# Performance work log

Hardware: AMD Instinct MI355X
Metric: run time of the kernel (lower is better)

## Reference

```python
import jax, jax.numpy as jnp
import numpy as np

D_MODEL = 768
NUM_HEADS = 12
D_K = D_MODEL // NUM_HEADS
D_FF = 3072
EPS = 1e-5


def _layer_norm(x, gamma, beta):
    mu = jnp.mean(x, axis=-1, keepdims=True)
    var = jnp.mean(jnp.square(x - mu), axis=-1, keepdims=True)
    return (x - mu) * jax.lax.rsqrt(var + EPS) * gamma + beta


def setup_inputs() -> dict:
    key = jax.random.key(0)
    ks = jax.random.split(key, 16)
    s = 1.0 / np.sqrt(D_MODEL)
    sf = 1.0 / np.sqrt(D_FF)
    inp = {
        "x": jax.random.normal(ks[0], (2, 2048, D_MODEL), dtype=jnp.float32),
        "Wq": jax.random.uniform(ks[1], (D_MODEL, D_MODEL), jnp.float32, -s, s),
        "bq": jax.random.uniform(ks[2], (D_MODEL,), jnp.float32, -s, s),
        "Wk": jax.random.uniform(ks[3], (D_MODEL, D_MODEL), jnp.float32, -s, s),
        "bk": jax.random.uniform(ks[4], (D_MODEL,), jnp.float32, -s, s),
        "Wv": jax.random.uniform(ks[5], (D_MODEL, D_MODEL), jnp.float32, -s, s),
        "bv": jax.random.uniform(ks[6], (D_MODEL,), jnp.float32, -s, s),
        "Wo": jax.random.uniform(ks[7], (D_MODEL, D_MODEL), jnp.float32, -s, s),
        "bo": jax.random.uniform(ks[8], (D_MODEL,), jnp.float32, -s, s),
        "W1": jax.random.uniform(ks[9], (D_MODEL, D_FF), jnp.float32, -s, s),
        "b1": jax.random.uniform(ks[10], (D_FF,), jnp.float32, -s, s),
        "W2": jax.random.uniform(ks[11], (D_FF, D_MODEL), jnp.float32, -sf, sf),
        "b2": jax.random.uniform(ks[12], (D_MODEL,), jnp.float32, -sf, sf),
        "g1": jnp.ones((D_MODEL,), jnp.float32),
        "be1": jnp.zeros((D_MODEL,), jnp.float32),
        "g2": jnp.ones((D_MODEL,), jnp.float32),
        "be2": jnp.zeros((D_MODEL,), jnp.float32),
    }
    return inp


def reference(x, Wq, bq, Wk, bk, Wv, bv, Wo, bo, W1, b1, W2, b2, g1, be1, g2, be2):
    B, S, _ = x.shape

    def split(h):  # (B,S,D) -> (B,H,S,Dk)
        return h.reshape(B, S, NUM_HEADS, D_K).transpose(0, 2, 1, 3)

    q = split(x @ Wq + bq)
    k = split(x @ Wk + bk)
    v = split(x @ Wv + bv)

    # naive attention: materialize full (B,H,S,S) scores as in the original
    scores = jnp.einsum("bhsd,bhtd->bhst", q, k) / np.sqrt(D_K)
    attn = jax.nn.softmax(scores, axis=-1)
    ctx = jnp.einsum("bhst,bhtd->bhsd", attn, v)
    ctx = ctx.transpose(0, 2, 1, 3).reshape(B, S, D_MODEL)
    attn_out = ctx @ Wo + bo

    x = _layer_norm(x + attn_out, g1, be1)
    ff = jax.nn.relu(x @ W1 + b1) @ W2 + b2
    x = _layer_norm(x + ff, g2, be2)
    return x
```

## Files before the change

### kernel.cpp

```cpp
#include <hip/hip_runtime.h>
#include <cstdint>


typedef unsigned short u16;
typedef unsigned int u32;
typedef __attribute__((ext_vector_type(4))) float f32x4;
typedef __attribute__((ext_vector_type(8))) short s16x8;
typedef __attribute__((ext_vector_type(4))) u16  u16x4;
typedef __attribute__((ext_vector_type(2))) u32  u32x2;

#define AS1 __attribute__((address_space(1)))
#define AS3 __attribute__((address_space(3)))

__device__ __forceinline__ u16 f2b(float f) {
  union { float f; unsigned u; } v; v.f = f;
  unsigned r = v.u + 0x7FFFu + ((v.u >> 16) & 1u);
  return (u16)(r >> 16);
}

__device__ __forceinline__ float b2f(u16 v) {
  union { float f; u32 u; } x; x.u = ((u32)v) << 16; return x.f;
}

__device__ __forceinline__ void gl_lds16(const void* g, void* lds_uniform_base) {
  __builtin_amdgcn_global_load_lds((const AS1 void*)g, (AS3 void*)lds_uniform_base, 16, 0, 0);
}

__device__ __forceinline__ f32x4 mfma16(s16x8 a, s16x8 b, f32x4 c) {
  return __builtin_amdgcn_mfma_f32_16x16x32_bf16(a, b, c, 0, 0, 0);
}

__device__ __forceinline__ u32 cvt_pk_bf16(float lo, float hi) {
  u32 r;
  asm("v_cvt_pk_bf16_f32 %0, %1, %2" : "=v"(r) : "v"(lo), "v"(hi));
  return r;
}

__device__ __forceinline__ float max3f(float a, float b, float c) {
  return fmaxf(fmaxf(a, b), c);
}

__device__ __forceinline__ void block_barrier() {
  asm volatile("" ::: "memory");
  __builtin_amdgcn_s_barrier();
  asm volatile("" ::: "memory");
}

__global__ __launch_bounds__(256) void prep(
    const float* __restrict__ Wq, const float* __restrict__ Wk,
    const float* __restrict__ Wv, const float* __restrict__ Wo,
    const float* __restrict__ W1, const float* __restrict__ W2,
    const float* __restrict__ bq, const float* __restrict__ bk,
    const float* __restrict__ bv, const float* __restrict__ x,
    u16* __restrict__ Wqkv_t, u16* __restrict__ Wo_t,
    u16* __restrict__ W1_t, u16* __restrict__ W2_t,
    float* __restrict__ bqkv, u16* __restrict__ Xb, int convBlocks) {
  __shared__ float ts[32][33];
  const int bid = blockIdx.x;
  const int tx = threadIdx.x, ty = threadIdx.y;
  if (bid < 6912) {
    const float* W; u16* Wt; int K, N, tile;
    if (bid < 2304) {
      int w = bid / 576; tile = bid - w * 576; K = 768; N = 768;
      W = (w == 0) ? Wq : (w == 1) ? Wk : (w == 2) ? Wv : Wo;
      Wt = (w < 3) ? Wqkv_t + (size_t)w * 768 * 768 : Wo_t;
    } else if (bid < 4608) {
      tile = bid - 2304; K = 768; N = 3072; W = W1; Wt = W1_t;
    } else {
      tile = bid - 4608; K = 3072; N = 768; W = W2; Wt = W2_t;
    }
    int ntx = N >> 5;
    int n0 = (tile % ntx) * 32, k0 = (tile / ntx) * 32;
#pragma unroll
    for (int yy = 0; yy < 32; yy += 8)
      ts[ty + yy][tx] = W[(size_t)(k0 + ty + yy) * N + n0 + tx];
    __syncthreads();
#pragma unroll
    for (int yy = 0; yy < 32; yy += 8)
      Wt[(size_t)(n0 + ty + yy) * K + k0 + tx] = f2b(ts[tx][ty + yy]);
  } else if (bid < 6912 + convBlocks) {
    int t = ty * 32 + tx;
    size_t i = ((size_t)(bid - 6912) * 256 + t) * 4;
    f32x4 v = *(const f32x4*)(x + i);
    u16x4 o;
#pragma unroll
    for (int k = 0; k < 4; ++k) o[k] = f2b(v[k]);
    *(u16x4*)(Xb + i) = o;
  } else {
    int t = ty * 32 + tx;
    int i = (bid - 6912 - convBlocks) * 256 + t;
    if (i < 2304) bqkv[i] = (i < 768) ? bq[i] : (i < 1536) ? bk[i - 768] : bv[i - 1536];
  }
}

__global__ __launch_bounds__(256) void transpose_v(const u16* __restrict__ Vh,
                                                   u16* __restrict__ Vt) {
  __shared__ u16 tile[32][33];
  int bh = blockIdx.z;
  int d0 = blockIdx.x * 32, s0 = blockIdx.y * 32;
  const u16* src = Vh + (size_t)bh * 2048 * 64;
  u16* dst = Vt + (size_t)bh * 64 * 2048;
  int x = threadIdx.x, y = threadIdx.y;
#pragma unroll
  for (int yy = 0; yy < 32; yy += 8)
    tile[y + yy][x] = src[(size_t)(s0 + y + yy) * 64 + d0 + x];
  __syncthreads();
#pragma unroll
  for (int yy = 0; yy < 32; yy += 8)
    dst[(size_t)(d0 + y + yy) * 2048 + s0 + x] = tile[x][y + yy];
}

template <int MODE>
__global__ __launch_bounds__(256) void gemm_bt(const u16* __restrict__ A,
                                               const u16* __restrict__ Bt,
                                               const float* __restrict__ bias,
                                               float* __restrict__ Cf, u16* __restrict__ Cb,
                                               u16* __restrict__ Qo, u16* __restrict__ Ko,
                                               u16* __restrict__ Vo, int M, int N, int K,
                                               int Klen) {
  __shared__ __align__(16) u16 lsA[2][128 * 64];
  __shared__ __align__(16) u16 lsB[2][128 * 64];
  const int tid = threadIdx.x;
  const int lane = tid & 63, wave = tid >> 6;
  const int lr = lane & 15, lh = lane >> 4;
  const int wr = wave >> 1, wc = wave & 1;

  int bx, by, bz;
  {
    int nx = gridDim.x, ny = gridDim.y, nz = gridDim.z;
    int total = nx * ny * nz;
    int lin = blockIdx.x + nx * (blockIdx.y + ny * blockIdx.z);
    if ((total & 7) == 0) {
      int key = (lin & 7) * (total >> 3) + (lin >> 3);
      by = key % ny;
      int t2 = key / ny;
      bz = t2 % nz;
      bx = t2 / nz;
    } else {
      bx = blockIdx.x; by = blockIdx.y; bz = blockIdx.z;
    }
  }
  const int m0 = by * 128;
  const int n0 = bx * 128;
  const int kB = bz * Klen;

  f32x4 acc[4][4];
#pragma unroll
  for (int i = 0; i < 4; ++i)
#pragma unroll
    for (int j = 0; j < 4; ++j) acc[i][j] = f32x4{0.f, 0.f, 0.f, 0.f};

  const size_t aBase = (size_t)m0 * K;
  const size_t bBase = (size_t)n0 * K;
  const int srow8 = tid >> 3;
  const int scolE = (((tid & 7) * 16) ^ ((srow8 & 7) << 4)) >> 1;
  const int xk = (lr & 7) << 4;

  auto stage = [&](int buf, int kt) {
#pragma unroll
    for (int i = 0; i < 4; ++i) {
      int row = i * 32 + srow8;
      int ldsOff = buf * 16384 + i * 4096 + wave * 1024;
      gl_lds16(A + aBase + (size_t)row * K + kt + scolE, (char*)lsA + ldsOff);
      gl_lds16(Bt + bBase + (size_t)row * K + kt + scolE, (char*)lsB + ldsOff);
    }
  };

  const int nk = Klen >> 6;
  stage(0, kB);
  for (int t = 0; t < nk; ++t) {
    const int cur = t & 1;
    if (t + 1 < nk) {
      stage(cur ^ 1, kB + (t + 1) * 64);
      asm volatile("s_waitcnt vmcnt(8)" ::: "memory");
    } else {
      asm volatile("s_waitcnt vmcnt(0)" ::: "memory");
    }
    block_barrier();
    const char* baA = (const char*)lsA + cur * 16384;
    const char* baB = (const char*)lsB + cur * 16384;
#pragma unroll
    for (int ks = 0; ks < 2; ++ks) {
      int cb = (ks * 64 + lh * 16) ^ xk;
      s16x8 a[4], b[4];
#pragma unroll
      for (int i = 0; i < 4; ++i) {
        a[i] = *(const s16x8*)(baA + (wr * 64 + i * 16 + lr) * 128 + cb);
        b[i] = *(const s16x8*)(baB + (wc * 64 + i * 16 + lr) * 128 + cb);
      }
#pragma unroll
      for (int i = 0; i < 4; ++i)
#pragma unroll
        for (int j = 0; j < 4; ++j) acc[i][j] = mfma16(a[i], b[j], acc[i][j]);
    }
    block_barrier();
  }

  float* CfP = Cf + (size_t)bz * M * N;
#pragma unroll
  for (int i = 0; i < 4; ++i) {
    int growb = m0 + wr * 64 + i * 16 + lh * 4;
#pragma unroll
    for (int j = 0; j < 4; ++j) {
      int col = n0 + wc * 64 + j * 16 + lr;
      float bv = (MODE != 0 || bz == 0) ? bias[col] : 0.f;
#pragma unroll
      for (int q = 0; q < 4; ++q) {
        int grow = growb + q;
        float v = acc[i][j][q] + bv;
        if (MODE == 0) {
          CfP[(size_t)grow * N + col] = v;
        } else if (MODE == 1) {
          Cb[(size_t)grow * N + col] = f2b(fmaxf(v, 0.f));
        } else {
          int sel = col / 768;
          int c2 = col - sel * 768;
          int h = c2 >> 6, d = c2 & 63;
          int b = grow >> 11, s = grow & 2047;
          size_t idx = (((size_t)(b * 12 + h)) * 2048 + s) * 64 + d;
          float vv = (sel == 0) ? v * 0.1803368801f : v;
          u16* dst = (sel == 0) ? Qo : (sel == 1) ? Ko : Vo;
          dst[idx] = f2b(vv);
        }
      }
    }
  }
}

__global__ __launch_bounds__(512) void attn(const u16* __restrict__ Qh,
                                            const u16* __restrict__ Kh,
                                            const u16* __restrict__ Vt,
                                            u16* __restrict__ Opb,
                                            float* __restrict__ ml,
                                            int nbh, int ntile) {
  __shared__ __align__(16) u16 lsK[2][64 * 64];
  __shared__ __align__(16) u16 lsV[2][64 * 64];
  __shared__ __align__(16) u16 lsP[8][16 * 64];
  const int tid = threadIdx.x, lane = tid & 63, wave = tid >> 6;
  const int lr = lane & 15, lh = lane >> 4;

  int bx = blockIdx.x, bh = blockIdx.y, z = blockIdx.z;
  {
    int nz = gridDim.z;
    int total = 16 * nbh * nz;
    if ((total & 7) == 0) {
      int lin = bx + 16 * (bh + nbh * z);
      int nl = (lin & 7) * (total >> 3) + (lin >> 3);
      bx = nl & 15;
      bh = (nl >> 4) % nbh;
      z = nl / (16 * nbh);
    }
  }
  const int q0 = bx * 128 + wave * 16;
  const size_t kvBase = (size_t)bh * 2048 * 64;
  const int tB = z * ntile;

  const int srow = tid >> 3;
  const int scol = (((tid & 7) * 16) ^ ((srow & 7) << 4)) >> 1;
  const u16* kSrcBase = Kh + kvBase + (size_t)srow * 64 + scol;
  const u16* vSrcBase = Vt + kvBase + (size_t)srow * 2048 + scol;

  s16x8 qf[2];
#pragma unroll
  for (int ks = 0; ks < 2; ++ks)
    qf[ks] = *(const s16x8*)(Qh + kvBase + (size_t)(q0 + lr) * 64 + ks * 32 + lh * 8);

  s16x8 onesf;
#pragma unroll
  for (int k = 0; k < 8; ++k) onesf[k] = (short)0x3F80;

  f32x4 oacc[4];
  f32x4 aOnes = f32x4{0.f, 0.f, 0.f, 0.f};
  float mrow = -1e30f;
#pragma unroll
  for (int d = 0; d < 4; ++d) oacc[d] = f32x4{0.f, 0.f, 0.f, 0.f};

  gl_lds16(kSrcBase + (size_t)tB * 4096, (char*)lsK[0] + wave * 1024);
  gl_lds16(vSrcBase + tB * 64,           (char*)lsV[0] + wave * 1024);

  for (int it = 0; it < ntile; ++it) {
    const int cur = it & 1;
    __syncthreads();

    s16x8 kb[2][4];
#pragma unroll
    for (int ks = 0; ks < 2; ++ks)
#pragma unroll
      for (int j = 0; j < 4; ++j) {
        int r = j * 16 + lr;
        kb[ks][j] = *(const s16x8*)((const char*)lsK[cur] + r * 128 +
                                    ((ks * 64 + lh * 16) ^ ((r & 7) << 4)));
      }

    if (it + 1 < ntile) {
      int t = tB + it + 1;
      gl_lds16(kSrcBase + (size_t)t * 4096, (char*)lsK[cur ^ 1] + wave * 1024);
      gl_lds16(vSrcBase + t * 64,           (char*)lsV[cur ^ 1] + wave * 1024);
    }

    f32x4 st[4];
#pragma unroll
    for (int j = 0; j < 4; ++j) st[j] = f32x4{0.f, 0.f, 0.f, 0.f};
    __builtin_amdgcn_s_setprio(1);
#pragma unroll
    for (int ks = 0; ks < 2; ++ks)
#pragma unroll
      for (int j = 0; j < 4; ++j) st[j] = mfma16(kb[ks][j], qf[ks], st[j]);
    __builtin_amdgcn_s_setprio(0);

    float mx;
    {
      float t0 = max3f(st[0][0], st[0][1], st[0][2]);
      float t1 = max3f(st[0][3], st[1][0], st[1][1]);
      float t2 = max3f(st[1][2], st[1][3], st[2][0]);
      float t3 = max3f(st[2][1], st[2][2], st[2][3]);
      float t4 = max3f(st[3][0], st[3][1], st[3][2]);
      mx = fmaxf(max3f(t0, t1, t2), max3f(t3, t4, st[3][3]));
      mx = fmaxf(mx, __shfl_xor(mx, 16));
      mx = fmaxf(mx, __shfl_xor(mx, 32));
    }
    if (__any(mx > mrow + 11.f)) {
      float mn = fmaxf(mrow, mx);
      float al = exp2f(mrow - mn);
      mrow = mn;
#pragma unroll
      for (int q = 0; q < 4; ++q) aOnes[q] *= al;
#pragma unroll
      for (int d = 0; d < 4; ++d)
#pragma unroll
        for (int q = 0; q < 4; ++q) oacc[d][q] *= al;
    }

#pragma unroll
    for (int j = 0; j < 4; ++j) {
      float p0 = exp2f(st[j][0] - mrow);
      float p1 = exp2f(st[j][1] - mrow);
      float p2 = exp2f(st[j][2] - mrow);
      float p3 = exp2f(st[j][3] - mrow);
      u32x2 pk;
      pk.x = cvt_pk_bf16(p0, p1);
      pk.y = cvt_pk_bf16(p2, p3);
      *(u32x2*)((char*)lsP[wave] + lr * 128 + ((j * 32 + lh * 8) ^ ((lr & 7) << 4))) = pk;
    }

    __builtin_amdgcn_s_setprio(1);
#pragma unroll
    for (int ks = 0; ks < 2; ++ks) {
      s16x8 pa = *(const s16x8*)((const char*)lsP[wave] + lr * 128 +
                                 ((ks * 64 + lh * 16) ^ ((lr & 7) << 4)));
      aOnes = mfma16(onesf, pa, aOnes);
#pragma unroll
      for (int d = 0; d < 4; ++d) {
        int r = d * 16 + lr;
        s16x8 vb = *(const s16x8*)((const char*)lsV[cur] + r * 128 +
                                   ((ks * 64 + lh * 16) ^ ((r & 7) << 4)));
        oacc[d] = mfma16(vb, pa, oacc[d]);
      }
    }
    __builtin_amdgcn_s_setprio(0);
  }

  {
    int s = q0 + lr;
    size_t r = ((size_t)z * nbh + bh) * 2048 + s;
#pragma unroll
    for (int d = 0; d < 4; ++d) {
      u32x2 pk;
      pk.x = cvt_pk_bf16(oacc[d][0], oacc[d][1]);
      pk.y = cvt_pk_bf16(oacc[d][2], oacc[d][3]);
      *(u32x2*)(Opb + r * 64 + d * 16 + lh * 4) = pk;
    }
    if (lh == 0) { ml[r * 2] = mrow; ml[r * 2 + 1] = aOnes[0]; }
  }
}

template <int NZ>
__global__ __launch_bounds__(256) void attn_combine(const u16* __restrict__ Opb,
                                                    const float* __restrict__ ml,
                                                    u16* __restrict__ ctx, int nbh) {
  size_t i = (size_t)blockIdx.x * 256 + threadIdx.x;
  int d4 = (int)(i & 15);
  size_t rs = i >> 4;
  size_t zs = (size_t)nbh * 2048;
  float m[NZ], l[NZ];
  float mx = -1e30f;
#pragma unroll
  for (int p = 0; p < NZ; ++p) {
    m[p] = ml[(p * zs + rs) * 2];
    l[p] = ml[(p * zs + rs) * 2 + 1];
    mx = fmaxf(mx, m[p]);
  }
  float wsum = 0.f, a[NZ];
#pragma unroll
  for (int p = 0; p < NZ; ++p) { a[p] = exp2f(m[p] - mx); wsum += l[p] * a[p]; }
  float inv = 1.f / wsum;
  f32x4 o = f32x4{0.f, 0.f, 0.f, 0.f};
#pragma unroll
  for (int p = 0; p < NZ; ++p) {
    u16x4 op = *(const u16x4*)(Opb + (p * zs + rs) * 64 + d4 * 4);
#pragma unroll
    for (int k = 0; k < 4; ++k) o[k] += b2f(op[k]) * a[p];
  }
  int bh = (int)(rs >> 11), s = (int)(rs & 2047);
  int b = bh / 12, h = bh - b * 12;
  u16x4 r;
#pragma unroll
  for (int k = 0; k < 4; ++k) r[k] = f2b(o[k] * inv);
  *(u16x4*)(ctx + ((size_t)(b * 2048 + s)) * 768 + h * 64 + d4 * 4) = r;
}

template <int NP>
__global__ __launch_bounds__(256) void resid_ln(const float* __restrict__ xin,
                                                const float* __restrict__ yp,
                                                size_t pstride,
                                                const float* __restrict__ gamma,
                                                const float* __restrict__ beta,
                                                float* __restrict__ outf,
                                                u16* __restrict__ outb) {
  const int row = blockIdx.x, t = threadIdx.x;
  const size_t base4 = (size_t)row * 192;
  const bool act = t < 192;
  f32x4 v = f32x4{0.f, 0.f, 0.f, 0.f};
  float s = 0.f, s2 = 0.f;
  if (act) {
    v = ((const f32x4*)xin)[base4 + t];
#pragma unroll
    for (int p = 0; p < NP; ++p) {
      f32x4 y = ((const f32x4*)(yp + p * pstride))[base4 + t];
#pragma unroll
      for (int k = 0; k < 4; ++k) v[k] += y[k];
    }
    s = (v[0] + v[1]) + (v[2] + v[3]);
    s2 = (v[0] * v[0] + v[1] * v[1]) + (v[2] * v[2] + v[3] * v[3]);
  }
#pragma unroll
  for (int off = 32; off > 0; off >>= 1) {
    s += __shfl_down(s, off, 64);
    s2 += __shfl_down(s2, off, 64);
  }
  __shared__ float red[8];
  int lane = t & 63, wave = t >> 6;
  if (lane == 0) { red[wave] = s; red[4 + wave] = s2; }
  __syncthreads();
  s = red[0] + red[1] + red[2] + red[3];
  s2 = red[4] + red[5] + red[6] + red[7];
  const float inv = 1.f / 768.f;
  float mu = s * inv;
  float var = fmaxf(s2 * inv - mu * mu, 0.f);
  float rs = rsqrtf(var + 1e-5f);
  if (act) {
    f32x4 g = ((const f32x4*)gamma)[t];
    f32x4 bb = ((const f32x4*)beta)[t];
    f32x4 o;
#pragma unroll
    for (int k = 0; k < 4; ++k) o[k] = (v[k] - mu) * rs * g[k] + bb[k];
    if (outf) ((f32x4*)outf)[base4 + t] = o;
    if (outb) {
      u16x4 ob;
#pragma unroll
      for (int k = 0; k < 4; ++k) ob[k] = f2b(o[k]);
      ((u16x4*)outb)[base4 + t] = ob;
    }
  }
}

extern "C" void kernel_launch(void* const* d_in, const int* in_sizes, int n_in,
                              void* d_out, int out_size, void* d_ws, size_t ws_size,
                              hipStream_t stream) {
  const float* x   = (const float*)d_in[0];
  const float* Wq  = (const float*)d_in[1];
  const float* bq  = (const float*)d_in[2];
  const float* Wk  = (const float*)d_in[3];
  const float* bk  = (const float*)d_in[4];
  const float* Wv  = (const float*)d_in[5];
  const float* bv  = (const float*)d_in[6];
  const float* Wo  = (const float*)d_in[7];
  const float* bo  = (const float*)d_in[8];
  const float* W1  = (const float*)d_in[9];
  const float* b1  = (const float*)d_in[10];
  const float* W2  = (const float*)d_in[11];
  const float* b2  = (const float*)d_in[12];
  const float* g1  = (const float*)d_in[13];
  const float* be1 = (const float*)d_in[14];
  const float* g2  = (const float*)d_in[15];
  const float* be2 = (const float*)d_in[16];
  float* out = (float*)d_out;

  const int M = in_sizes[0] / 768;
  const int B = M / 2048;
  const int nbh = B * 12;

  char* ws = (char*)d_ws;
  size_t off = 0;
  auto alloc = [&](size_t bytes) -> void* {
    void* p = ws + off;
    off += (bytes + 255) & ~(size_t)255;
    return p;
  };
  u16*   Wqkv_t = (u16*)alloc((size_t)2304 * 768 * 2);
  u16*   Wo_t   = (u16*)alloc((size_t)768 * 768 * 2);
  u16*   W1_t   = (u16*)alloc((size_t)3072 * 768 * 2);
  u16*   W2_t   = (u16*)alloc((size_t)768 * 3072 * 2);
  float* bqkv   = (float*)alloc(2304 * 4);
  u16*   Xb     = (u16*)alloc((size_t)M * 768 * 2);
  u16*   Qh     = (u16*)alloc((size_t)M * 768 * 2);
  u16*   Kh     = (u16*)alloc((size_t)M * 768 * 2);
  u16*   Vh     = (u16*)alloc((size_t)M * 768 * 2);
  u16*   Vt     = (u16*)alloc((size_t)M * 768 * 2);

  size_t pstride = (size_t)M * 768;
  size_t fixedRest = pstride * 4  + pstride * 2  +
                     (size_t)M * 3072 * 2  + 4096;
  const int ZSPLIT = 2;
  size_t opElems = (size_t)ZSPLIT * nbh * 2048 * 64;
  size_t attnBytes = opElems * 2 + (size_t)ZSPLIT * nbh * 2048 * 2 * 4;
  size_t reg4 = attnBytes > pstride * 16 ? attnBytes : pstride * 16;
  int FSPLIT;
  size_t regionBytes;
  if (off + reg4 + fixedRest <= ws_size) {
    FSPLIT = 4; regionBytes = reg4;
  } else {
    FSPLIT = 2;
    regionBytes = attnBytes > pstride * 8 ? attnBytes : pstride * 8;
  }
  float* region = (float*)alloc(regionBytes);
  u16*   Opb  = (u16*)region;
  float* ml   = (float*)((char*)region + opElems * 2);
  float* ffnPart  = region;
  float* projPart = (float*)Qh;
  float* x1f  = (float*)alloc(pstride * 4);
  u16*   x1b  = (u16*)alloc(pstride * 2);
  u16*   hb   = (u16*)alloc((size_t)M * 3072 * 2);
  u16*   ctx  = Xb;

  dim3 tb(32, 8);
  const int convBlocks = (M * 768) / 1024;
  prep<<<6912 + convBlocks + 9, tb, 0, stream>>>(
      Wq, Wk, Wv, Wo, W1, W2, bq, bk, bv, x,
      Wqkv_t, Wo_t, W1_t, W2_t, bqkv, Xb, convBlocks);

  gemm_bt<2><<<dim3(2304 / 128, M / 128), 256, 0, stream>>>(
      Xb, Wqkv_t, bqkv, nullptr, nullptr, Qh, Kh, Vh, M, 2304, 768, 768);

  transpose_v<<<dim3(2, 64, nbh), tb, 0, stream>>>(Vh, Vt);

  attn<<<dim3(16, nbh, ZSPLIT), 512, 0, stream>>>(Qh, Kh, Vt, Opb, ml, nbh, 32 / ZSPLIT);
  attn_combine<2><<<nbh * 128, 256, 0, stream>>>(Opb, ml, ctx, nbh);

  gemm_bt<0><<<dim3(768 / 128, M / 128, 2), 256, 0, stream>>>(
      ctx, Wo_t, bo, projPart, nullptr, nullptr, nullptr, nullptr, M, 768, 768, 384);

  resid_ln<2><<<M, 256, 0, stream>>>(x, projPart, pstride, g1, be1, x1f, x1b);

  gemm_bt<1><<<dim3(3072 / 128, M / 128), 256, 0, stream>>>(
      x1b, W1_t, b1, nullptr, hb, nullptr, nullptr, nullptr, M, 3072, 768, 768);

  if (FSPLIT == 4) {
    gemm_bt<0><<<dim3(768 / 128, M / 128, 4), 256, 0, stream>>>(
        hb, W2_t, b2, ffnPart, nullptr, nullptr, nullptr, nullptr, M, 768, 3072, 768);
    resid_ln<4><<<M, 256, 0, stream>>>(x1f, ffnPart, pstride, g2, be2, out, nullptr);
  } else {
    gemm_bt<0><<<dim3(768 / 128, M / 128, 2), 256, 0, stream>>>(
        hb, W2_t, b2, ffnPart, nullptr, nullptr, nullptr, nullptr, M, 768, 3072, 1536);
    resid_ln<2><<<M, 256, 0, stream>>>(x1f, ffnPart, pstride, g2, be2, out, nullptr);
  }
}
```

Baseline: 210.6 us.

## Fuse V transpose into QKV GEMM epilogue and store split-K partials as bf16

The QKV GEMM epilogue now writes V directly in transposed per-head layout as 4-element vector stores, which removes the separate transpose_v kernel and the Vh buffer. The split-K partial outputs of the Wo and W2 GEMMs are stored as bf16 instead of fp32, and resid_ln reads them back as bf16. This halves the partial-sum traffic, at the cost of precision loss in the residual sums.

Result: faster. 202.5 us (median of 2 runs) (-3.8%).

```diff
diff --git a/kernel.cpp b/kernel.cpp
--- a/kernel.cpp
+++ b/kernel.cpp
@@ -93,30 +93,13 @@
   }
 }
 
-__global__ __launch_bounds__(256) void transpose_v(const u16* __restrict__ Vh,
-                                                   u16* __restrict__ Vt) {
-  __shared__ u16 tile[32][33];
-  int bh = blockIdx.z;
-  int d0 = blockIdx.x * 32, s0 = blockIdx.y * 32;
-  const u16* src = Vh + (size_t)bh * 2048 * 64;
-  u16* dst = Vt + (size_t)bh * 64 * 2048;
-  int x = threadIdx.x, y = threadIdx.y;
-#pragma unroll
-  for (int yy = 0; yy < 32; yy += 8)
-    tile[y + yy][x] = src[(size_t)(s0 + y + yy) * 64 + d0 + x];
-  __syncthreads();
-#pragma unroll
-  for (int yy = 0; yy < 32; yy += 8)
-    dst[(size_t)(d0 + y + yy) * 2048 + s0 + x] = tile[x][y + yy];
-}
-
 template <int MODE>
 __global__ __launch_bounds__(256) void gemm_bt(const u16* __restrict__ A,
                                                const u16* __restrict__ Bt,
                                                const float* __restrict__ bias,
-                                               float* __restrict__ Cf, u16* __restrict__ Cb,
+                                               u16* __restrict__ Cb,
                                                u16* __restrict__ Qo, u16* __restrict__ Ko,
-                                               u16* __restrict__ Vo, int M, int N, int K,
+                                               u16* __restrict__ Vt, int M, int N, int K,
                                                int Klen) {
   __shared__ __align__(16) u16 lsA[2][128 * 64];
   __shared__ __align__(16) u16 lsB[2][128 * 64];
@@ -196,7 +179,7 @@
     block_barrier();
   }
 
-  float* CfP = Cf + (size_t)bz * M * N;
+  u16* CbP = Cb + (size_t)bz * M * N;
 #pragma unroll
   for (int i = 0; i < 4; ++i) {
     int growb = m0 + wr * 64 + i * 16 + lh * 4;
@@ -204,23 +187,36 @@
     for (int j = 0; j < 4; ++j) {
       int col = n0 + wc * 64 + j * 16 + lr;
       float bv = (MODE != 0 || bz == 0) ? bias[col] : 0.f;
-#pragma unroll
-      for (int q = 0; q < 4; ++q) {
-        int grow = growb + q;
-        float v = acc[i][j][q] + bv;
-        if (MODE == 0) {
-          CfP[(size_t)grow * N + col] = v;
-        } else if (MODE == 1) {
-          Cb[(size_t)grow * N + col] = f2b(fmaxf(v, 0.f));
+      if (MODE == 2) {
+        int sel = col / 768;
+        int c2 = col - sel * 768;
+        int h = c2 >> 6, d = c2 & 63;
+        int b = growb >> 11, s0 = growb & 2047;
+        if (sel == 2) {
+          u16x4 ob;
+#pragma unroll
+          for (int q = 0; q < 4; ++q) ob[q] = f2b(acc[i][j][q] + bv);
+          *(u16x4*)(Vt + (((size_t)(b * 12 + h)) * 64 + d) * 2048 + s0) = ob;
         } else {
-          int sel = col / 768;
-          int c2 = col - sel * 768;
-          int h = c2 >> 6, d = c2 & 63;
-          int b = grow >> 11, s = grow & 2047;
-          size_t idx = (((size_t)(b * 12 + h)) * 2048 + s) * 64 + d;
-          float vv = (sel == 0) ? v * 0.1803368801f : v;
-          u16* dst = (sel == 0) ? Qo : (sel == 1) ? Ko : Vo;
-          dst[idx] = f2b(vv);
+#pragma unroll
+          for (int q = 0; q < 4; ++q) {
+            float v = acc[i][j][q] + bv;
+            size_t idx = (((size_t)(b * 12 + h)) * 2048 + (s0 + q)) * 64 + d;
+            float vv = (sel == 0) ? v * 0.1803368801f : v;
+            u16* dst = (sel == 0) ? Qo : Ko;
+            dst[idx] = f2b(vv);
+          }
+        }
+      } else {
+#pragma unroll
+        for (int q = 0; q < 4; ++q) {
+          int grow = growb + q;
+          float v = acc[i][j][q] + bv;
+          if (MODE == 0) {
+            CbP[(size_t)grow * N + col] = f2b(v);
+          } else {
+            Cb[(size_t)grow * N + col] = f2b(fmaxf(v, 0.f));
+          }
         }
       }
     }
@@ -411,7 +407,7 @@
 
 template <int NP>
 __global__ __launch_bounds__(256) void resid_ln(const float* __restrict__ xin,
-                                                const float* __restrict__ yp,
+                                                const u16* __restrict__ yp,
                                                 size_t pstride,
                                                 const float* __restrict__ gamma,
                                                 const float* __restrict__ beta,
@@ -426,9 +422,9 @@
     v = ((const f32x4*)xin)[base4 + t];
 #pragma unroll
     for (int p = 0; p < NP; ++p) {
-      f32x4 y = ((const f32x4*)(yp + p * pstride))[base4 + t];
-#pragma unroll
-      for (int k = 0; k < 4; ++k) v[k] += y[k];
+      u16x4 y = *(const u16x4*)(yp + p * pstride + (size_t)row * 768 + t * 4);
+#pragma unroll
+      for (int k = 0; k < 4; ++k) v[k] += b2f(y[k]);
     }
     s = (v[0] + v[1]) + (v[2] + v[3]);
     s2 = (v[0] * v[0] + v[1] * v[1]) + (v[2] * v[2] + v[3] * v[3]);
@@ -505,7 +501,6 @@
   u16*   Xb     = (u16*)alloc((size_t)M * 768 * 2);
   u16*   Qh     = (u16*)alloc((size_t)M * 768 * 2);
   u16*   Kh     = (u16*)alloc((size_t)M * 768 * 2);
-  u16*   Vh     = (u16*)alloc((size_t)M * 768 * 2);
   u16*   Vt     = (u16*)alloc((size_t)M * 768 * 2);
 
   size_t pstride = (size_t)M * 768;
@@ -514,20 +509,21 @@
   const int ZSPLIT = 2;
   size_t opElems = (size_t)ZSPLIT * nbh * 2048 * 64;
   size_t attnBytes = opElems * 2 + (size_t)ZSPLIT * nbh * 2048 * 2 * 4;
-  size_t reg4 = attnBytes > pstride * 16 ? attnBytes : pstride * 16;
+  size_t reg4 = attnBytes;
+  if (reg4 < pstride * 2 * 4) reg4 = pstride * 2 * 4;
   int FSPLIT;
   size_t regionBytes;
   if (off + reg4 + fixedRest <= ws_size) {
     FSPLIT = 4; regionBytes = reg4;
   } else {
     FSPLIT = 2;
-    regionBytes = attnBytes > pstride * 8 ? attnBytes : pstride * 8;
+    regionBytes = attnBytes > pstride * 2 * 2 ? attnBytes : pstride * 2 * 2;
   }
   float* region = (float*)alloc(regionBytes);
   u16*   Opb  = (u16*)region;
   float* ml   = (float*)((char*)region + opElems * 2);
-  float* ffnPart  = region;
-  float* projPart = (float*)Qh;
+  u16*   projPart = (u16*)region;
+  u16*   ffnPart  = (u16*)region;
   float* x1f  = (float*)alloc(pstride * 4);
   u16*   x1b  = (u16*)alloc(pstride * 2);
   u16*   hb   = (u16*)alloc((size_t)M * 3072 * 2);
@@ -540,28 +536,26 @@
       Wqkv_t, Wo_t, W1_t, W2_t, bqkv, Xb, convBlocks);
 
   gemm_bt<2><<<dim3(2304 / 128, M / 128), 256, 0, stream>>>(
-      Xb, Wqkv_t, bqkv, nullptr, nullptr, Qh, Kh, Vh, M, 2304, 768, 768);
-
-  transpose_v<<<dim3(2, 64, nbh), tb, 0, stream>>>(Vh, Vt);
+      Xb, Wqkv_t, bqkv, nullptr, Qh, Kh, Vt, M, 2304, 768, 768);
 
   attn<<<dim3(16, nbh, ZSPLIT), 512, 0, stream>>>(Qh, Kh, Vt, Opb, ml, nbh, 32 / ZSPLIT);
   attn_combine<2><<<nbh * 128, 256, 0, stream>>>(Opb, ml, ctx, nbh);
 
   gemm_bt<0><<<dim3(768 / 128, M / 128, 2), 256, 0, stream>>>(
-      ctx, Wo_t, bo, projPart, nullptr, nullptr, nullptr, nullptr, M, 768, 768, 384);
+      ctx, Wo_t, bo, projPart, nullptr, nullptr, nullptr, M, 768, 768, 384);
 
   resid_ln<2><<<M, 256, 0, stream>>>(x, projPart, pstride, g1, be1, x1f, x1b);
 
   gemm_bt<1><<<dim3(3072 / 128, M / 128), 256, 0, stream>>>(
-      x1b, W1_t, b1, nullptr, hb, nullptr, nullptr, nullptr, M, 3072, 768, 768);
+      x1b, W1_t, b1, hb, nullptr, nullptr, nullptr, M, 3072, 768, 768);
 
   if (FSPLIT == 4) {
     gemm_bt<0><<<dim3(768 / 128, M / 128, 4), 256, 0, stream>>>(
-        hb, W2_t, b2, ffnPart, nullptr, nullptr, nullptr, nullptr, M, 768, 3072, 768);
+        hb, W2_t, b2, ffnPart, nullptr, nullptr, nullptr, M, 768, 3072, 768);
     resid_ln<4><<<M, 256, 0, stream>>>(x1f, ffnPart, pstride, g2, be2, out, nullptr);
   } else {
     gemm_bt<0><<<dim3(768 / 128, M / 128, 2), 256, 0, stream>>>(
-        hb, W2_t, b2, ffnPart, nullptr, nullptr, nullptr, nullptr, M, 768, 3072, 1536);
+        hb, W2_t, b2, ffnPart, nullptr, nullptr, nullptr, M, 768, 3072, 1536);
     resid_ln<2><<<M, 256, 0, stream>>>(x1f, ffnPart, pstride, g2, be2, out, nullptr);
   }
 }
```
